# Kernel tuning notes

Measured on AMD Instinct MI355X. Metric: run time of the kernel, lower is better.

Reference implementation:

```python
import jax, jax.numpy as jnp
import numpy as np

N_FEATURES = 16384
N_EXPERTS = 8
D_IN = 768
EXPERT_DIM = N_FEATURES // N_EXPERTS  # 2048
N_TOKENS = 16384


def setup_inputs() -> dict:
    key = jax.random.key(0)
    k_act, k_preb, k_enc, k_dec, k_rb, k_r = jax.random.split(key, 6)
    activations = jax.random.normal(k_act, (N_TOKENS, D_IN), dtype=jnp.float32)
    pre_b = jax.random.normal(k_preb, (D_IN,), dtype=jnp.float32) * 0.01
    enc = jax.random.normal(k_enc, (N_EXPERTS, D_IN, EXPERT_DIM), dtype=jnp.float32) / (2.0 ** 0.5) / (D_IN ** 0.5)
    dec = jax.random.normal(k_dec, (N_EXPERTS, EXPERT_DIM, D_IN), dtype=jnp.float32) / (EXPERT_DIM ** 0.5)
    router_b = jax.random.normal(k_rb, (D_IN,), dtype=jnp.float32) * 0.01
    router = jax.random.normal(k_r, (D_IN, N_EXPERTS), dtype=jnp.float32) / (D_IN ** 0.5)
    return {"activations": activations, "pre_b": pre_b, "enc": enc, "dec": dec,
            "router_b": router_b, "router": router}


def reference(activations, pre_b, enc, dec, router_b, router):
    # Router: softmax over experts, top-1 routing.
    logits = (activations - router_b) @ router            # [N, E]
    probs = jax.nn.softmax(logits, axis=-1)
    expert_max_prob = jnp.max(probs, axis=-1)              # [N]
    expert_idx = jnp.argmax(probs, axis=-1)                # [N] int

    n_experts = enc.shape[0]
    recons = jnp.zeros_like(activations)
    # Fixed small loop over experts; tokens are masked (zeroed) per expert so
    # each per-expert encode/decode GEMM only contributes for its routed rows.
    for e in range(n_experts):
        mask = (expert_idx == e)[:, None]                  # [N, 1]
        x_e = jnp.where(mask, activations, 0.0)            # masked gather
        latent = jax.nn.relu(x_e @ enc[e])                 # [N, expert_dim]
        recon = latent @ dec[e]                            # [N, d_in]
        recons = recons + jnp.where(mask, recon, 0.0)      # scatter-combine

    return expert_max_prob[:, None] * recons + pre_b
```

## Files before the change

kernel.cpp:

```cpp
#include <hip/hip_runtime.h>
#include <hip/hip_bf16.h>
#include <hip/hip_fp16.h>

#define N_TOKENS 16384
#define D_IN 768
#define N_EXPERTS 8
#define EXPERT_DIM 2048

#define ROUTER_BLOCKS 256
#define TOK_PER_BLOCK 64

typedef _Float16 half8 __attribute__((ext_vector_type(8)));
typedef _Float16 half4 __attribute__((ext_vector_type(4)));
typedef float floatx4 __attribute__((ext_vector_type(4)));

#define GBM 256
#define GBK 64

#define WAIT_VM0 0xF70

__device__ __forceinline__ void glds16(const _Float16* g, _Float16* l) {
    __builtin_amdgcn_global_load_lds(
        (const __attribute__((address_space(1))) unsigned int*)g,
        (__attribute__((address_space(3))) unsigned int*)l, 16, 0, 0);
}

__global__ __launch_bounds__(256) void router_convert(const float* __restrict__ act,
    const float* __restrict__ router_b, const float* __restrict__ router,
    _Float16* __restrict__ act_h, float* __restrict__ prob, int* __restrict__ localpos,
    int* __restrict__ eidx, int* __restrict__ hist)
{
    __shared__ int h[N_EXPERTS];
    if (threadIdx.x < N_EXPERTS) h[threadIdx.x] = 0;
    __syncthreads();

    int wave = threadIdx.x >> 6, lane = threadIdx.x & 63;

    float rb[3][4];
#pragma unroll
    for (int c = 0; c < 3; ++c) {
        float4 v = *(const float4*)(router_b + lane * 4 + c * 256);
        rb[c][0] = v.x; rb[c][1] = v.y; rb[c][2] = v.z; rb[c][3] = v.w;
    }

#pragma unroll 1
    for (int it = 0; it < 16; ++it) {
        int t = blockIdx.x * TOK_PER_BLOCK + wave * 16 + it;
        const float* arow = act + (size_t)t * D_IN;
        float acc[8];
#pragma unroll
        for (int e = 0; e < 8; ++e) acc[e] = 0.f;
#pragma unroll
        for (int c = 0; c < 3; ++c) {
            int i0 = lane * 4 + c * 256;
            float4 v = *(const float4*)(arow + i0);
            half4 hv;
            hv[0] = (_Float16)v.x; hv[1] = (_Float16)v.y;
            hv[2] = (_Float16)v.z; hv[3] = (_Float16)v.w;
            *(half4*)(act_h + (size_t)t * D_IN + i0) = hv;
            float va[4] = {v.x, v.y, v.z, v.w};
#pragma unroll
            for (int q = 0; q < 4; ++q) {
                float a = va[q] - rb[c][q];
                const float* r = router + (size_t)(i0 + q) * 8;
#pragma unroll
                for (int e = 0; e < 8; ++e) acc[e] += a * r[e];
            }
        }
#pragma unroll
        for (int s = 32; s > 0; s >>= 1) {
#pragma unroll
            for (int e = 0; e < 8; ++e) acc[e] += __shfl_down(acc[e], s, 64);
        }
        if (lane == 0) {
            float m = acc[0]; int ai = 0;
#pragma unroll
            for (int e = 1; e < 8; ++e) if (acc[e] > m) { m = acc[e]; ai = e; }
            float s = 0.f;
#pragma unroll
            for (int e = 0; e < 8; ++e) s += __expf(acc[e] - m);
            prob[t] = 1.0f / s;
            eidx[t] = ai;
            localpos[t] = atomicAdd(&h[ai], 1);
        }
    }
    __syncthreads();
    if (threadIdx.x < N_EXPERTS) hist[blockIdx.x * N_EXPERTS + threadIdx.x] = h[threadIdx.x];
}

__global__ __launch_bounds__(256) void scan_kernel(int* __restrict__ hist,
    int* __restrict__ counts, int* __restrict__ offsets)
{
    __shared__ int sh[ROUTER_BLOCKS * N_EXPERTS];
    __shared__ int tot[N_EXPERTS], off[N_EXPERTS];
    int tid = threadIdx.x;
    *(int4*)&sh[tid * 8]     = *(const int4*)&hist[tid * 8];
    *(int4*)&sh[tid * 8 + 4] = *(const int4*)&hist[tid * 8 + 4];
    __syncthreads();
    if (tid < N_EXPERTS) {
        int run = 0;
        for (int b = 0; b < ROUTER_BLOCKS; ++b) {
            int v = sh[b * 8 + tid];
            sh[b * 8 + tid] = run;
            run += v;
        }
        tot[tid] = run;
    }
    __syncthreads();
    if (tid == 0) {
        int run = 0;
        for (int e = 0; e < N_EXPERTS; ++e) {
            off[e] = run; offsets[e] = run; counts[e] = tot[e]; run += tot[e];
        }
    }
    __syncthreads();
    int4 a = *(const int4*)&sh[tid * 8];
    int4 b = *(const int4*)&sh[tid * 8 + 4];
    a.x += off[0]; a.y += off[1]; a.z += off[2]; a.w += off[3];
    b.x += off[4]; b.y += off[5]; b.z += off[6]; b.w += off[7];
    *(int4*)&hist[tid * 8]     = a;
    *(int4*)&hist[tid * 8 + 4] = b;
}

__global__ __launch_bounds__(256) void order_kernel(const int* __restrict__ eidx,
    const int* __restrict__ localpos, const int* __restrict__ hist,
    int* __restrict__ order)
{
    int t = blockIdx.x * 256 + threadIdx.x;
    int base = hist[(t >> 6) * N_EXPERTS + eidx[t]];
    order[base + localpos[t]] = t;
}

__global__ __launch_bounds__(256) void transpose_to_half(const float* __restrict__ W,
    _Float16* __restrict__ WT, int K, int Nc)
{
    __shared__ _Float16 tile[64][72];
    size_t esz = (size_t)K * Nc;
    const float* We = W + (size_t)blockIdx.z * esz;
    _Float16* WTe = WT + (size_t)blockIdx.z * esz;
    int n0 = blockIdx.x * 64, k0 = blockIdx.y * 64;
    int tr = threadIdx.x >> 4;
    int tc = threadIdx.x & 15;
#pragma unroll
    for (int rr = 0; rr < 64; rr += 16) {
        int k = k0 + rr + tr;
        float4 v = *(const float4*)(We + (size_t)k * Nc + n0 + tc * 4);
        tile[tc * 4 + 0][rr + tr] = (_Float16)v.x;
        tile[tc * 4 + 1][rr + tr] = (_Float16)v.y;
        tile[tc * 4 + 2][rr + tr] = (_Float16)v.z;
        tile[tc * 4 + 3][rr + tr] = (_Float16)v.w;
    }
    __syncthreads();
#pragma unroll
    for (int p = 0; p < 2; ++p) {
        int id = threadIdx.x + p * 256;
        int r = id >> 3, ch = id & 7;
        half8 v = *(const half8*)&tile[r][ch * 8];
        *(half8*)(WTe + (size_t)(n0 + r) * K + k0 + ch * 8) = v;
    }
}

__global__ __launch_bounds__(512, 2) void encode_kernel(const _Float16* __restrict__ act_h,
    const _Float16* __restrict__ encT, const int* __restrict__ order,
    const int* __restrict__ counts, const int* __restrict__ offsets,
    _Float16* __restrict__ latent)
{
    int id = blockIdx.x;
    int e = id & 7;
    int j = id >> 3;
    int nt = j & 7;
    int mt = j >> 3;

    int n_e = counts[e];
    if (mt * GBM >= n_e) return;
    int slot0 = offsets[e] + mt * GBM;
    int mrem = n_e - mt * GBM;

    __shared__ _Float16 lds[2][32768];
    __shared__ int s_tok[GBM];

    int tid = threadIdx.x;
    if (tid < GBM) s_tok[tid] = (tid < mrem) ? order[slot0 + tid] : order[slot0];
    __syncthreads();

    int w = tid >> 6, lane = tid & 63;
    int wm = w >> 2, wn = w & 3;
    int mrow = lane & 15;

    int st_dst = w * 512 + lane * 8;
    int c_st = ((lane & 7) - (lane >> 3)) & 7;
    int row_st = w * 8 + (lane >> 3);
    const _Float16* Be = encT + (size_t)e * D_IN * EXPERT_DIM + (size_t)(nt * 256) * D_IN;
    const _Float16* pa0 = act_h + (size_t)s_tok[0 * 64 + row_st] * D_IN + c_st * 8;
    const _Float16* pa1 = act_h + (size_t)s_tok[1 * 64 + row_st] * D_IN + c_st * 8;
    const _Float16* pa2 = act_h + (size_t)s_tok[2 * 64 + row_st] * D_IN + c_st * 8;
    const _Float16* pa3 = act_h + (size_t)s_tok[3 * 64 + row_st] * D_IN + c_st * 8;
    const _Float16* pb0 = Be + (size_t)(0 * 64 + row_st) * D_IN + c_st * 8;
    const _Float16* pb1 = Be + (size_t)(1 * 64 + row_st) * D_IN + c_st * 8;
    const _Float16* pb2 = Be + (size_t)(2 * 64 + row_st) * D_IN + c_st * 8;
    const _Float16* pb3 = Be + (size_t)(3 * 64 + row_st) * D_IN + c_st * 8;

    int c0 = ((lane >> 4) + (lane & 7)) & 7;
    int aoff0 = (wm * 128 + mrow) * 64 + c0 * 8;
    int aoff1 = (wm * 128 + mrow) * 64 + (c0 ^ 4) * 8;
    int boff0 = 16384 + (wn * 64 + mrow) * 64 + c0 * 8;
    int boff1 = 16384 + (wn * 64 + mrow) * 64 + (c0 ^ 4) * 8;

#define ENC_STAGE(bufp, k0h)                                           \
    do {                                                               \
        glds16(pa0 + (k0h), (bufp) + 0 * 4096 + st_dst);               \
        glds16(pa1 + (k0h), (bufp) + 1 * 4096 + st_dst);               \
        glds16(pa2 + (k0h), (bufp) + 2 * 4096 + st_dst);               \
        glds16(pa3 + (k0h), (bufp) + 3 * 4096 + st_dst);               \
        glds16(pb0 + (k0h), (bufp) + 16384 + 0 * 4096 + st_dst);       \
        glds16(pb1 + (k0h), (bufp) + 16384 + 1 * 4096 + st_dst);       \
        glds16(pb2 + (k0h), (bufp) + 16384 + 2 * 4096 + st_dst);       \
        glds16(pb3 + (k0h), (bufp) + 16384 + 3 * 4096 + st_dst);       \
    } while (0)

    floatx4 acc[8][4];
#pragma unroll
    for (int i = 0; i < 8; ++i)
#pragma unroll
        for (int jj = 0; jj < 4; ++jj) acc[i][jj] = (floatx4){0.f, 0.f, 0.f, 0.f};

    const int T = D_IN / GBK;
    ENC_STAGE(&lds[0][0], 0);
    __builtin_amdgcn_s_waitcnt(WAIT_VM0);
    __builtin_amdgcn_s_barrier();

#pragma unroll 1
    for (int t = 0; t < T; ++t) {
        _Float16* cur = &lds[t & 1][0];
        if (t + 1 < T) {
            _Float16* nxt = &lds[(t + 1) & 1][0];
            ENC_STAGE(nxt, (t + 1) * GBK);
        }
        half8 a0[8], b0[4];
#pragma unroll
        for (int i = 0; i < 8; ++i) a0[i] = *(const half8*)&cur[aoff0 + i * 1024];
#pragma unroll
        for (int jj = 0; jj < 4; ++jj) b0[jj] = *(const half8*)&cur[boff0 + jj * 1024];
        __builtin_amdgcn_s_setprio(1);
#pragma unroll
        for (int i = 0; i < 8; ++i)
#pragma unroll
            for (int jj = 0; jj < 4; ++jj)
                acc[i][jj] = __builtin_amdgcn_mfma_f32_16x16x32_f16(a0[i], b0[jj], acc[i][jj], 0, 0, 0);
        __builtin_amdgcn_s_setprio(0);
        half8 a1[8], b1[4];
#pragma unroll
        for (int i = 0; i < 8; ++i) a1[i] = *(const half8*)&cur[aoff1 + i * 1024];
#pragma unroll
        for (int jj = 0; jj < 4; ++jj) b1[jj] = *(const half8*)&cur[boff1 + jj * 1024];
        __builtin_amdgcn_s_setprio(1);
#pragma unroll
        for (int i = 0; i < 8; ++i)
#pragma unroll
            for (int jj = 0; jj < 4; ++jj)
                acc[i][jj] = __builtin_amdgcn_mfma_f32_16x16x32_f16(a1[i], b1[jj], acc[i][jj], 0, 0, 0);
        __builtin_amdgcn_s_setprio(0);
        if (t + 1 < T) {
            __builtin_amdgcn_s_waitcnt(WAIT_VM0);
            __builtin_amdgcn_s_barrier();
        }
    }
#undef ENC_STAGE

#pragma unroll
    for (int i = 0; i < 8; ++i) {
        int row0 = wm * 128 + i * 16 + (lane >> 4) * 4;
#pragma unroll
        for (int jj = 0; jj < 4; ++jj) {
            int col = nt * 256 + wn * 64 + jj * 16 + mrow;
#pragma unroll
            for (int r = 0; r < 4; ++r) {
                int row = row0 + r;
                if (row < mrem) {
                    float v = acc[i][jj][r];
                    v = v > 0.f ? v : 0.f;
                    latent[(size_t)(slot0 + row) * EXPERT_DIM + col] = (_Float16)v;
                }
            }
        }
    }
}

__global__ __launch_bounds__(512, 2) void decode_kernel(const _Float16* __restrict__ latent,
    const _Float16* __restrict__ decT, const int* __restrict__ order,
    const int* __restrict__ counts, const int* __restrict__ offsets,
    const float* __restrict__ prob, const float* __restrict__ pre_b,
    float* __restrict__ out)
{
    int id = blockIdx.x;
    int e = id & 7;
    int j = id >> 3;
    int nt = j & 3;
    int mt = j >> 2;

    int n_e = counts[e];
    if (mt * GBM >= n_e) return;
    int slot0 = offsets[e] + mt * GBM;
    int mrem = n_e - mt * GBM;

    __shared__ _Float16 lds[2][28672];
    __shared__ int s_tok[GBM];
    __shared__ float s_p[GBM];

    int tid = threadIdx.x;
    if (tid < GBM) {
        int tok = (tid < mrem) ? order[slot0 + tid] : order[slot0];
        s_tok[tid] = tok;
        s_p[tid] = prob[tok];
    }
    __syncthreads();

    int w = tid >> 6, lane = tid & 63;
    int wm = w >> 2, wn = w & 3;
    int mrow = lane & 15;

    int st_dst = w * 512 + lane * 8;
    int c_st = ((lane & 7) - (lane >> 3)) & 7;
    int row_st = w * 8 + (lane >> 3);
    const _Float16* Ae = latent + (size_t)slot0 * EXPERT_DIM;
    const _Float16* Be = decT + (size_t)e * EXPERT_DIM * D_IN + (size_t)(nt * 192) * EXPERT_DIM;
    const _Float16* pa0 = Ae + (size_t)(0 * 64 + row_st) * EXPERT_DIM + c_st * 8;
    const _Float16* pa1 = Ae + (size_t)(1 * 64 + row_st) * EXPERT_DIM + c_st * 8;
    const _Float16* pa2 = Ae + (size_t)(2 * 64 + row_st) * EXPERT_DIM + c_st * 8;
    const _Float16* pa3 = Ae + (size_t)(3 * 64 + row_st) * EXPERT_DIM + c_st * 8;
    const _Float16* pb0 = Be + (size_t)(0 * 64 + row_st) * EXPERT_DIM + c_st * 8;
    const _Float16* pb1 = Be + (size_t)(1 * 64 + row_st) * EXPERT_DIM + c_st * 8;
    const _Float16* pb2 = Be + (size_t)(2 * 64 + row_st) * EXPERT_DIM + c_st * 8;

    int c0 = ((lane >> 4) + (lane & 7)) & 7;
    int aoff0 = (wm * 128 + mrow) * 64 + c0 * 8;
    int aoff1 = (wm * 128 + mrow) * 64 + (c0 ^ 4) * 8;
    int boff0 = 16384 + (wn * 48 + mrow) * 64 + c0 * 8;
    int boff1 = 16384 + (wn * 48 + mrow) * 64 + (c0 ^ 4) * 8;

#define DEC_STAGE(bufp, k0h)                                           \
    do {                                                               \
        glds16(pa0 + (k0h), (bufp) + 0 * 4096 + st_dst);               \
        glds16(pa1 + (k0h), (bufp) + 1 * 4096 + st_dst);               \
        glds16(pa2 + (k0h), (bufp) + 2 * 4096 + st_dst);               \
        glds16(pa3 + (k0h), (bufp) + 3 * 4096 + st_dst);               \
        glds16(pb0 + (k0h), (bufp) + 16384 + 0 * 4096 + st_dst);       \
        glds16(pb1 + (k0h), (bufp) + 16384 + 1 * 4096 + st_dst);       \
        glds16(pb2 + (k0h), (bufp) + 16384 + 2 * 4096 + st_dst);       \
    } while (0)

    floatx4 acc[8][3];
#pragma unroll
    for (int i = 0; i < 8; ++i)
#pragma unroll
        for (int jj = 0; jj < 3; ++jj) acc[i][jj] = (floatx4){0.f, 0.f, 0.f, 0.f};

    const int T = EXPERT_DIM / GBK;
    DEC_STAGE(&lds[0][0], 0);
    __builtin_amdgcn_s_waitcnt(WAIT_VM0);
    __builtin_amdgcn_s_barrier();

#pragma unroll 1
    for (int t = 0; t < T; ++t) {
        _Float16* cur = &lds[t & 1][0];
        if (t + 1 < T) {
            _Float16* nxt = &lds[(t + 1) & 1][0];
            DEC_STAGE(nxt, (t + 1) * GBK);
        }
        half8 a0[8], b0[3];
#pragma unroll
        for (int i = 0; i < 8; ++i) a0[i] = *(const half8*)&cur[aoff0 + i * 1024];
#pragma unroll
        for (int jj = 0; jj < 3; ++jj) b0[jj] = *(const half8*)&cur[boff0 + jj * 1024];
        __builtin_amdgcn_s_setprio(1);
#pragma unroll
        for (int i = 0; i < 8; ++i)
#pragma unroll
            for (int jj = 0; jj < 3; ++jj)
                acc[i][jj] = __builtin_amdgcn_mfma_f32_16x16x32_f16(a0[i], b0[jj], acc[i][jj], 0, 0, 0);
        __builtin_amdgcn_s_setprio(0);
        half8 a1[8], b1[3];
#pragma unroll
        for (int i = 0; i < 8; ++i) a1[i] = *(const half8*)&cur[aoff1 + i * 1024];
#pragma unroll
        for (int jj = 0; jj < 3; ++jj) b1[jj] = *(const half8*)&cur[boff1 + jj * 1024];
        __builtin_amdgcn_s_setprio(1);
#pragma unroll
        for (int i = 0; i < 8; ++i)
#pragma unroll
            for (int jj = 0; jj < 3; ++jj)
                acc[i][jj] = __builtin_amdgcn_mfma_f32_16x16x32_f16(a1[i], b1[jj], acc[i][jj], 0, 0, 0);
        __builtin_amdgcn_s_setprio(0);
        if (t + 1 < T) {
            __builtin_amdgcn_s_waitcnt(WAIT_VM0);
            __builtin_amdgcn_s_barrier();
        }
    }
#undef DEC_STAGE

#pragma unroll
    for (int i = 0; i < 8; ++i) {
        int row0 = wm * 128 + i * 16 + (lane >> 4) * 4;
#pragma unroll
        for (int jj = 0; jj < 3; ++jj) {
            int col = nt * 192 + wn * 48 + jj * 16 + mrow;
            float pb = pre_b[col];
#pragma unroll
            for (int r = 0; r < 4; ++r) {
                int row = row0 + r;
                if (row < mrem) {
                    out[(size_t)s_tok[row] * D_IN + col] = s_p[row] * acc[i][jj][r] + pb;
                }
            }
        }
    }
}

extern "C" void kernel_launch(void* const* d_in, const int* in_sizes, int n_in,
                              void* d_out, int out_size, void* d_ws, size_t ws_size,
                              hipStream_t stream)
{
    const float* act      = (const float*)d_in[0];
    const float* pre_b    = (const float*)d_in[1];
    const float* enc      = (const float*)d_in[2];
    const float* dec      = (const float*)d_in[3];
    const float* router_b = (const float*)d_in[4];
    const float* router   = (const float*)d_in[5];
    float* out = (float*)d_out;

    char* w = (char*)d_ws;
    int* counts  = (int*)w;  w += 256;
    int* offsets = (int*)w;  w += 256;
    int* hist    = (int*)w;  w += ROUTER_BLOCKS * N_EXPERTS * 4;
    int* eidx    = (int*)w;  w += N_TOKENS * 4;
    int* lpos    = (int*)w;  w += N_TOKENS * 4;
    int* order   = (int*)w;  w += N_TOKENS * 4;
    float* prob  = (float*)w; w += N_TOKENS * 4;
    _Float16* act_h  = (_Float16*)w; w += (size_t)N_TOKENS * D_IN * 2;
    _Float16* encT   = (_Float16*)w; w += (size_t)N_EXPERTS * D_IN * EXPERT_DIM * 2;
    _Float16* decT   = (_Float16*)w; w += (size_t)N_EXPERTS * D_IN * EXPERT_DIM * 2;
    _Float16* latent = (_Float16*)w; w += (size_t)(N_TOKENS + GBM) * EXPERT_DIM * 2;

    router_convert<<<ROUTER_BLOCKS, 256, 0, stream>>>(act, router_b, router, act_h, prob, lpos, eidx, hist);
    scan_kernel<<<1, 256, 0, stream>>>(hist, counts, offsets);
    order_kernel<<<N_TOKENS / 256, 256, 0, stream>>>(eidx, lpos, hist, order);

    transpose_to_half<<<dim3(EXPERT_DIM / 64, D_IN / 64, N_EXPERTS), 256, 0, stream>>>(enc, encT, D_IN, EXPERT_DIM);
    transpose_to_half<<<dim3(D_IN / 64, EXPERT_DIM / 64, N_EXPERTS), 256, 0, stream>>>(dec, decT, EXPERT_DIM, D_IN);

    encode_kernel<<<4096, 512, 0, stream>>>(act_h, encT, order, counts, offsets, latent);
    decode_kernel<<<2048, 512, 0, stream>>>(latent, decT, order, counts, offsets, prob, pre_b, out);
}
```

Baseline: 403.2 us.

## Use 4-stage K=32 LDS pipeline and 256-wide decode tiles

Both GEMM kernels drop the double-buffered K=64 stages for a four-buffer ring of K=32 stages with three loads in flight, using partial vmcnt waits so global-to-LDS loads overlap more MFMA work. The LDS swizzle and staging addressing are reworked for the 32-wide rows. The decode kernel switches from 192-column N tiles to 256-column tiles (3 N tiles per expert instead of 4), which reuses each A tile over more columns but launches fewer blocks. The trade-off is an extra barrier per iteration, more barriers overall with half-size K steps, and the same LDS footprint.

```diff
diff --git a/kernel.cpp b/kernel.cpp
--- a/kernel.cpp
+++ b/kernel.cpp
@@ -14,10 +14,11 @@
 typedef _Float16 half4 __attribute__((ext_vector_type(4)));
 typedef float floatx4 __attribute__((ext_vector_type(4)));
 
-#define GBM 256
-#define GBK 64
-
-#define WAIT_VM0 0xF70
+
+#define WAIT_VM12 0xF7C
+#define WAIT_VM8  0xF78
+#define WAIT_VM4  0xF74
+#define WAIT_VM0  0xF70
 
 __device__ __forceinline__ void glds16(const _Float16* g, _Float16* l) {
     __builtin_amdgcn_global_load_lds(
@@ -160,6 +161,14 @@
     }
 }
 
+#define STAGE(bufp, k0h)                                        \
+    do {                                                        \
+        glds16(pa0 + (k0h), (bufp) + st_base);                  \
+        glds16(pa1 + (k0h), (bufp) + st_base + 512);            \
+        glds16(pb0 + (k0h), (bufp) + 8192 + st_base);           \
+        glds16(pb1 + (k0h), (bufp) + 8192 + st_base + 512);     \
+    } while (0)
+
 __global__ __launch_bounds__(512, 2) void encode_kernel(const _Float16* __restrict__ act_h,
     const _Float16* __restrict__ encT, const int* __restrict__ order,
     const int* __restrict__ counts, const int* __restrict__ offsets,
@@ -172,51 +181,33 @@
     int mt = j >> 3;
 
     int n_e = counts[e];
-    if (mt * GBM >= n_e) return;
-    int slot0 = offsets[e] + mt * GBM;
-    int mrem = n_e - mt * GBM;
-
-    __shared__ _Float16 lds[2][32768];
-    __shared__ int s_tok[GBM];
+    if (mt * 256 >= n_e) return;
+    int slot0 = offsets[e] + mt * 256;
+    int mrem = n_e - mt * 256;
+
+    __shared__ _Float16 lds[4][16384];
+    __shared__ int s_tok[256];
 
     int tid = threadIdx.x;
-    if (tid < GBM) s_tok[tid] = (tid < mrem) ? order[slot0 + tid] : order[slot0];
+    if (tid < 256) s_tok[tid] = (tid < mrem) ? order[slot0 + tid] : order[slot0];
     __syncthreads();
 
     int w = tid >> 6, lane = tid & 63;
     int wm = w >> 2, wn = w & 3;
     int mrow = lane & 15;
 
-    int st_dst = w * 512 + lane * 8;
-    int c_st = ((lane & 7) - (lane >> 3)) & 7;
-    int row_st = w * 8 + (lane >> 3);
+    int st_base = w * 1024 + lane * 8;
+    int c_st = ((lane & 3) - ((lane >> 3) & 3)) & 3;
+    int r_in = lane >> 2;
     const _Float16* Be = encT + (size_t)e * D_IN * EXPERT_DIM + (size_t)(nt * 256) * D_IN;
-    const _Float16* pa0 = act_h + (size_t)s_tok[0 * 64 + row_st] * D_IN + c_st * 8;
-    const _Float16* pa1 = act_h + (size_t)s_tok[1 * 64 + row_st] * D_IN + c_st * 8;
-    const _Float16* pa2 = act_h + (size_t)s_tok[2 * 64 + row_st] * D_IN + c_st * 8;
-    const _Float16* pa3 = act_h + (size_t)s_tok[3 * 64 + row_st] * D_IN + c_st * 8;
-    const _Float16* pb0 = Be + (size_t)(0 * 64 + row_st) * D_IN + c_st * 8;
-    const _Float16* pb1 = Be + (size_t)(1 * 64 + row_st) * D_IN + c_st * 8;
-    const _Float16* pb2 = Be + (size_t)(2 * 64 + row_st) * D_IN + c_st * 8;
-    const _Float16* pb3 = Be + (size_t)(3 * 64 + row_st) * D_IN + c_st * 8;
-
-    int c0 = ((lane >> 4) + (lane & 7)) & 7;
-    int aoff0 = (wm * 128 + mrow) * 64 + c0 * 8;
-    int aoff1 = (wm * 128 + mrow) * 64 + (c0 ^ 4) * 8;
-    int boff0 = 16384 + (wn * 64 + mrow) * 64 + c0 * 8;
-    int boff1 = 16384 + (wn * 64 + mrow) * 64 + (c0 ^ 4) * 8;
-
-#define ENC_STAGE(bufp, k0h)                                           \
-    do {                                                               \
-        glds16(pa0 + (k0h), (bufp) + 0 * 4096 + st_dst);               \
-        glds16(pa1 + (k0h), (bufp) + 1 * 4096 + st_dst);               \
-        glds16(pa2 + (k0h), (bufp) + 2 * 4096 + st_dst);               \
-        glds16(pa3 + (k0h), (bufp) + 3 * 4096 + st_dst);               \
-        glds16(pb0 + (k0h), (bufp) + 16384 + 0 * 4096 + st_dst);       \
-        glds16(pb1 + (k0h), (bufp) + 16384 + 1 * 4096 + st_dst);       \
-        glds16(pb2 + (k0h), (bufp) + 16384 + 2 * 4096 + st_dst);       \
-        glds16(pb3 + (k0h), (bufp) + 16384 + 3 * 4096 + st_dst);       \
-    } while (0)
+    const _Float16* pa0 = act_h + (size_t)s_tok[w * 32 + r_in] * D_IN + c_st * 8;
+    const _Float16* pa1 = act_h + (size_t)s_tok[w * 32 + 16 + r_in] * D_IN + c_st * 8;
+    const _Float16* pb0 = Be + (size_t)(w * 32 + r_in) * D_IN + c_st * 8;
+    const _Float16* pb1 = Be + (size_t)(w * 32 + 16 + r_in) * D_IN + c_st * 8;
+
+    int fo = (((lane >> 4) + (mrow >> 1)) & 3) * 8;
+    int aoff = (wm * 128 + mrow) * 32 + fo;
+    int boff = 8192 + (wn * 64 + mrow) * 32 + fo;
 
     floatx4 acc[8][4];
 #pragma unroll
@@ -224,48 +215,39 @@
 #pragma unroll
         for (int jj = 0; jj < 4; ++jj) acc[i][jj] = (floatx4){0.f, 0.f, 0.f, 0.f};
 
-    const int T = D_IN / GBK;
-    ENC_STAGE(&lds[0][0], 0);
-    __builtin_amdgcn_s_waitcnt(WAIT_VM0);
-    __builtin_amdgcn_s_barrier();
+    const int T = D_IN / 32;
+    STAGE(&lds[0][0], 0);
+    STAGE(&lds[1][0], 32);
+    STAGE(&lds[2][0], 64);
 
 #pragma unroll 1
     for (int t = 0; t < T; ++t) {
-        _Float16* cur = &lds[t & 1][0];
-        if (t + 1 < T) {
-            _Float16* nxt = &lds[(t + 1) & 1][0];
-            ENC_STAGE(nxt, (t + 1) * GBK);
-        }
-        half8 a0[8], b0[4];
-#pragma unroll
-        for (int i = 0; i < 8; ++i) a0[i] = *(const half8*)&cur[aoff0 + i * 1024];
-#pragma unroll
-        for (int jj = 0; jj < 4; ++jj) b0[jj] = *(const half8*)&cur[boff0 + jj * 1024];
+        _Float16* cur = &lds[t & 3][0];
+        if (t + 3 < T) {
+            STAGE(&lds[(t + 3) & 3][0], (t + 3) * 32);
+            __builtin_amdgcn_s_waitcnt(WAIT_VM12);
+        } else if (t + 2 < T) {
+            __builtin_amdgcn_s_waitcnt(WAIT_VM8);
+        } else if (t + 1 < T) {
+            __builtin_amdgcn_s_waitcnt(WAIT_VM4);
+        } else {
+            __builtin_amdgcn_s_waitcnt(WAIT_VM0);
+        }
+        __builtin_amdgcn_s_barrier();
+        half8 af[8], bf[4];
+#pragma unroll
+        for (int i = 0; i < 8; ++i) af[i] = *(const half8*)&cur[aoff + i * 512];
+#pragma unroll
+        for (int jj = 0; jj < 4; ++jj) bf[jj] = *(const half8*)&cur[boff + jj * 512];
         __builtin_amdgcn_s_setprio(1);
 #pragma unroll
         for (int i = 0; i < 8; ++i)
 #pragma unroll
             for (int jj = 0; jj < 4; ++jj)
-                acc[i][jj] = __builtin_amdgcn_mfma_f32_16x16x32_f16(a0[i], b0[jj], acc[i][jj], 0, 0, 0);
+                acc[i][jj] = __builtin_amdgcn_mfma_f32_16x16x32_f16(af[i], bf[jj], acc[i][jj], 0, 0, 0);
         __builtin_amdgcn_s_setprio(0);
-        half8 a1[8], b1[4];
-#pragma unroll
-        for (int i = 0; i < 8; ++i) a1[i] = *(const half8*)&cur[aoff1 + i * 1024];
-#pragma unroll
-        for (int jj = 0; jj < 4; ++jj) b1[jj] = *(const half8*)&cur[boff1 + jj * 1024];
-        __builtin_amdgcn_s_setprio(1);
-#pragma unroll
-        for (int i = 0; i < 8; ++i)
-#pragma unroll
-            for (int jj = 0; jj < 4; ++jj)
-                acc[i][jj] = __builtin_amdgcn_mfma_f32_16x16x32_f16(a1[i], b1[jj], acc[i][jj], 0, 0, 0);
-        __builtin_amdgcn_s_setprio(0);
-        if (t + 1 < T) {
-            __builtin_amdgcn_s_waitcnt(WAIT_VM0);
-            __builtin_amdgcn_s_barrier();
-        }
-    }
-#undef ENC_STAGE
+        __builtin_amdgcn_s_barrier();
+    }
 
 #pragma unroll
     for (int i = 0; i < 8; ++i) {
@@ -295,20 +277,20 @@
     int id = blockIdx.x;
     int e = id & 7;
     int j = id >> 3;
-    int nt = j & 3;
-    int mt = j >> 2;
+    int nt = j % 3;
+    int mt = j / 3;
 
     int n_e = counts[e];
-    if (mt * GBM >= n_e) return;
-    int slot0 = offsets[e] + mt * GBM;
-    int mrem = n_e - mt * GBM;
-
-    __shared__ _Float16 lds[2][28672];
-    __shared__ int s_tok[GBM];
-    __shared__ float s_p[GBM];
+    if (mt * 256 >= n_e) return;
+    int slot0 = offsets[e] + mt * 256;
+    int mrem = n_e - mt * 256;
+
+    __shared__ _Float16 lds[4][16384];
+    __shared__ int s_tok[256];
+    __shared__ float s_p[256];
 
     int tid = threadIdx.x;
-    if (tid < GBM) {
+    if (tid < 256) {
         int tok = (tid < mrem) ? order[slot0 + tid] : order[slot0];
         s_tok[tid] = tok;
         s_p[tid] = prob[tok];
@@ -319,91 +301,66 @@
     int wm = w >> 2, wn = w & 3;
     int mrow = lane & 15;
 
-    int st_dst = w * 512 + lane * 8;
-    int c_st = ((lane & 7) - (lane >> 3)) & 7;
-    int row_st = w * 8 + (lane >> 3);
+    int st_base = w * 1024 + lane * 8;
+    int c_st = ((lane & 3) - ((lane >> 3) & 3)) & 3;
+    int r_in = lane >> 2;
     const _Float16* Ae = latent + (size_t)slot0 * EXPERT_DIM;
-    const _Float16* Be = decT + (size_t)e * EXPERT_DIM * D_IN + (size_t)(nt * 192) * EXPERT_DIM;
-    const _Float16* pa0 = Ae + (size_t)(0 * 64 + row_st) * EXPERT_DIM + c_st * 8;
-    const _Float16* pa1 = Ae + (size_t)(1 * 64 + row_st) * EXPERT_DIM + c_st * 8;
-    const _Float16* pa2 = Ae + (size_t)(2 * 64 + row_st) * EXPERT_DIM + c_st * 8;
-    const _Float16* pa3 = Ae + (size_t)(3 * 64 + row_st) * EXPERT_DIM + c_st * 8;
-    const _Float16* pb0 = Be + (size_t)(0 * 64 + row_st) * EXPERT_DIM + c_st * 8;
-    const _Float16* pb1 = Be + (size_t)(1 * 64 + row_st) * EXPERT_DIM + c_st * 8;
-    const _Float16* pb2 = Be + (size_t)(2 * 64 + row_st) * EXPERT_DIM + c_st * 8;
-
-    int c0 = ((lane >> 4) + (lane & 7)) & 7;
-    int aoff0 = (wm * 128 + mrow) * 64 + c0 * 8;
-    int aoff1 = (wm * 128 + mrow) * 64 + (c0 ^ 4) * 8;
-    int boff0 = 16384 + (wn * 48 + mrow) * 64 + c0 * 8;
-    int boff1 = 16384 + (wn * 48 + mrow) * 64 + (c0 ^ 4) * 8;
-
-#define DEC_STAGE(bufp, k0h)                                           \
-    do {                                                               \
-        glds16(pa0 + (k0h), (bufp) + 0 * 4096 + st_dst);               \
-        glds16(pa1 + (k0h), (bufp) + 1 * 4096 + st_dst);               \
-        glds16(pa2 + (k0h), (bufp) + 2 * 4096 + st_dst);               \
-        glds16(pa3 + (k0h), (bufp) + 3 * 4096 + st_dst);               \
-        glds16(pb0 + (k0h), (bufp) + 16384 + 0 * 4096 + st_dst);       \
-        glds16(pb1 + (k0h), (bufp) + 16384 + 1 * 4096 + st_dst);       \
-        glds16(pb2 + (k0h), (bufp) + 16384 + 2 * 4096 + st_dst);       \
-    } while (0)
-
-    floatx4 acc[8][3];
+    const _Float16* Be = decT + (size_t)e * EXPERT_DIM * D_IN + (size_t)(nt * 256) * EXPERT_DIM;
+    const _Float16* pa0 = Ae + (size_t)(w * 32 + r_in) * EXPERT_DIM + c_st * 8;
+    const _Float16* pa1 = Ae + (size_t)(w * 32 + 16 + r_in) * EXPERT_DIM + c_st * 8;
+    const _Float16* pb0 = Be + (size_t)(w * 32 + r_in) * EXPERT_DIM + c_st * 8;
+    const _Float16* pb1 = Be + (size_t)(w * 32 + 16 + r_in) * EXPERT_DIM + c_st * 8;
+
+    int fo = (((lane >> 4) + (mrow >> 1)) & 3) * 8;
+    int aoff = (wm * 128 + mrow) * 32 + fo;
+    int boff = 8192 + (wn * 64 + mrow) * 32 + fo;
+
+    floatx4 acc[8][4];
 #pragma unroll
     for (int i = 0; i < 8; ++i)
 #pragma unroll
-        for (int jj = 0; jj < 3; ++jj) acc[i][jj] = (floatx4){0.f, 0.f, 0.f, 0.f};
-
-    const int T = EXPERT_DIM / GBK;
-    DEC_STAGE(&lds[0][0], 0);
-    __builtin_amdgcn_s_waitcnt(WAIT_VM0);
-    __builtin_amdgcn_s_barrier();
+        for (int jj = 0; jj < 4; ++jj) acc[i][jj] = (floatx4){0.f, 0.f, 0.f, 0.f};
+
+    const int T = EXPERT_DIM / 32;
+    STAGE(&lds[0][0], 0);
+    STAGE(&lds[1][0], 32);
+    STAGE(&lds[2][0], 64);
 
 #pragma unroll 1
     for (int t = 0; t < T; ++t) {
-        _Float16* cur = &lds[t & 1][0];
-        if (t + 1 < T) {
-            _Float16* nxt = &lds[(t + 1) & 1][0];
-            DEC_STAGE(nxt, (t + 1) * GBK);
-        }
-        half8 a0[8], b0[3];
-#pragma unroll
-        for (int i = 0; i < 8; ++i) a0[i] = *(const half8*)&cur[aoff0 + i * 1024];
-#pragma unroll
-        for (int jj = 0; jj < 3; ++jj) b0[jj] = *(const half8*)&cur[boff0 + jj * 1024];
+        _Float16* cur = &lds[t & 3][0];
+        if (t + 3 < T) {
+            STAGE(&lds[(t + 3) & 3][0], (t + 3) * 32);
+            __builtin_amdgcn_s_waitcnt(WAIT_VM12);
+        } else if (t + 2 < T) {
+            __builtin_amdgcn_s_waitcnt(WAIT_VM8);
+        } else if (t + 1 < T) {
+            __builtin_amdgcn_s_waitcnt(WAIT_VM4);
+        } else {
+            __builtin_amdgcn_s_waitcnt(WAIT_VM0);
+        }
+        __builtin_amdgcn_s_barrier();
+        half8 af[8], bf[4];
+#pragma unroll
+        for (int i = 0; i < 8; ++i) af[i] = *(const half8*)&cur[aoff + i * 512];
+#pragma unroll
+        for (int jj = 0; jj < 4; ++jj) bf[jj] = *(const half8*)&cur[boff + jj * 512];
         __builtin_amdgcn_s_setprio(1);
 #pragma unroll
         for (int i = 0; i < 8; ++i)
 #pragma unroll
-            for (int jj = 0; jj < 3; ++jj)
-                acc[i][jj] = __builtin_amdgcn_mfma_f32_16x16x32_f16(a0[i], b0[jj], acc[i][jj], 0, 0, 0);
+            for (int jj = 0; jj < 4; ++jj)
+                acc[i][jj] = __builtin_amdgcn_mfma_f32_16x16x32_f16(af[i], bf[jj], acc[i][jj], 0, 0, 0);
         __builtin_amdgcn_s_setprio(0);
-        half8 a1[8], b1[3];
-#pragma unroll
-        for (int i = 0; i < 8; ++i) a1[i] = *(const half8*)&cur[aoff1 + i * 1024];
-#pragma unroll
-        for (int jj = 0; jj < 3; ++jj) b1[jj] = *(const half8*)&cur[boff1 + jj * 1024];
-        __builtin_amdgcn_s_setprio(1);
-#pragma unroll
-        for (int i = 0; i < 8; ++i)
-#pragma unroll
-            for (int jj = 0; jj < 3; ++jj)
-                acc[i][jj] = __builtin_amdgcn_mfma_f32_16x16x32_f16(a1[i], b1[jj], acc[i][jj], 0, 0, 0);
-        __builtin_amdgcn_s_setprio(0);
-        if (t + 1 < T) {
-            __builtin_amdgcn_s_waitcnt(WAIT_VM0);
-            __builtin_amdgcn_s_barrier();
-        }
-    }
-#undef DEC_STAGE
+        __builtin_amdgcn_s_barrier();
+    }
 
 #pragma unroll
     for (int i = 0; i < 8; ++i) {
         int row0 = wm * 128 + i * 16 + (lane >> 4) * 4;
 #pragma unroll
-        for (int jj = 0; jj < 3; ++jj) {
-            int col = nt * 192 + wn * 48 + jj * 16 + mrow;
+        for (int jj = 0; jj < 4; ++jj) {
+            int col = nt * 256 + wn * 64 + jj * 16 + mrow;
             float pb = pre_b[col];
 #pragma unroll
             for (int r = 0; r < 4; ++r) {
@@ -439,7 +396,7 @@
     _Float16* act_h  = (_Float16*)w; w += (size_t)N_TOKENS * D_IN * 2;
     _Float16* encT   = (_Float16*)w; w += (size_t)N_EXPERTS * D_IN * EXPERT_DIM * 2;
     _Float16* decT   = (_Float16*)w; w += (size_t)N_EXPERTS * D_IN * EXPERT_DIM * 2;
-    _Float16* latent = (_Float16*)w; w += (size_t)(N_TOKENS + GBM) * EXPERT_DIM * 2;
+    _Float16* latent = (_Float16*)w; w += (size_t)(N_TOKENS + 256) * EXPERT_DIM * 2;
 
     router_convert<<<ROUTER_BLOCKS, 256, 0, stream>>>(act, router_b, router, act_h, prob, lpos, eidx, hist);
     scan_kernel<<<1, 256, 0, stream>>>(hist, counts, offsets);
@@ -449,5 +406,5 @@
     transpose_to_half<<<dim3(D_IN / 64, EXPERT_DIM / 64, N_EXPERTS), 256, 0, stream>>>(dec, decT, EXPERT_DIM, D_IN);
 
     encode_kernel<<<4096, 512, 0, stream>>>(act_h, encT, order, counts, offsets, latent);
-    decode_kernel<<<2048, 512, 0, stream>>>(latent, decT, order, counts, offsets, prob, pre_b, out);
-}
+    decode_kernel<<<1536, 512, 0, stream>>>(latent, decT, order, counts, offsets, prob, pre_b, out);
+}
```

Measured after the change: 391.0 us. 3.0% less time.
